# Performance work log

Hardware: AMD Instinct MI355X
Metric: run time of the kernel (lower is better)

## Reference

```python
import jax, jax.numpy as jnp
import numpy as np


def setup_inputs() -> dict:
    key = jax.random.key(0)
    kx, ky = jax.random.split(key)
    B, N, M, D = 4, 8192, 8192, 3
    x = jax.random.normal(kx, (B, N, D), dtype=jnp.float32)
    y = jax.random.normal(ky, (B, M, D), dtype=jnp.float32)
    return {"x": x, "y": y}


def reference(x, y):
    # Pairwise squared distances: [B, N, M]
    x2 = jnp.sum(x * x, axis=-1)  # [B, N]
    y2 = jnp.sum(y * y, axis=-1)  # [B, M]
    xy = jnp.einsum("bnd,bmd->bnm", x, y)  # [B, N, M]
    d2 = x2[:, :, None] + y2[:, None, :] - 2.0 * xy
    # Chamfer: min over the other set in each direction
    min_xy = jnp.min(d2, axis=2)  # [B, N] nearest y for each x
    min_yx = jnp.min(d2, axis=1)  # [B, M] nearest x for each y
    return jnp.mean(min_xy) + jnp.mean(min_yx)
```

## Files before the change

### kernel.cpp

```cpp
#include <hip/hip_runtime.h>

#define BATCHES 4
#define NPTS    8192
#define INF32   3.0e38f

typedef _Float16 f16x8  __attribute__((ext_vector_type(8)));
typedef float    f32x16 __attribute__((ext_vector_type(16)));

__device__ inline void fsplit(float v, _Float16& h, _Float16& l) {
    h = (_Float16)v;
    l = (_Float16)(v - (float)h);
}

__device__ inline void pack_point(float p0, float p1, float p2,
                                  _Float16* __restrict__ avec,
                                  _Float16* __restrict__ bvec)
{
    _Float16 h[3], l[3];
    fsplit(p0, h[0], l[0]); fsplit(p1, h[1], l[1]); fsplit(p2, h[2], l[2]);
    float q = fmaf(p2, p2, fmaf(p1, p1, p0 * p0));
    _Float16 qh, ql;
    fsplit(q, qh, ql);

    __align__(16) _Float16 av[16];
    __align__(16) _Float16 bv[16];
    #pragma unroll
    for (int k = 0; k < 3; ++k) {
        av[k]     = h[k];
        av[3 + k] = l[k];
        av[6 + k] = h[k];
        bv[k]     = (_Float16)(-2.0f * (float)h[k]);
        bv[3 + k] = bv[k];
        bv[6 + k] = (_Float16)(-2.0f * (float)l[k]);
    }
    av[9] = qh; av[10] = ql; av[11] = (_Float16)1.0f; av[12] = (_Float16)1.0f;
    bv[9] = (_Float16)1.0f; bv[10] = (_Float16)1.0f; bv[11] = qh; bv[12] = ql;
    av[13] = av[14] = av[15] = (_Float16)0.0f;
    bv[13] = bv[14] = bv[15] = (_Float16)0.0f;

    ((int4*)avec)[0] = ((int4*)av)[0]; ((int4*)avec)[1] = ((int4*)av)[1];
    ((int4*)bvec)[0] = ((int4*)bv)[0]; ((int4*)bvec)[1] = ((int4*)bv)[1];
}

__global__ __launch_bounds__(256) void chamfer_prep(
    const float* __restrict__ x, const float* __restrict__ y,
    _Float16* __restrict__ pAx, _Float16* __restrict__ pBx,
    _Float16* __restrict__ pAy, _Float16* __restrict__ pBy,
    int* __restrict__ mininit )
{
    int i = blockIdx.x * 256 + threadIdx.x;
    mininit[i]         = 0x7F7F7F7F;
    mininit[i + 32768] = 0x7F7F7F7F;

    const float* xp = x + (size_t)i * 3;
    const float* yp = y + (size_t)i * 3;
    pack_point(xp[0], xp[1], xp[2], pAx + (size_t)i * 16, pBx + (size_t)i * 16);
    pack_point(yp[0], yp[1], yp[2], pAy + (size_t)i * 16, pBy + (size_t)i * 16);
}

__global__ __launch_bounds__(256, 4) void chamfer_mfma(
    const _Float16* __restrict__ pAx, const _Float16* __restrict__ pBx,
    const _Float16* __restrict__ pAy, const _Float16* __restrict__ pBy,
    float* __restrict__ minall )
{
    int bid   = blockIdx.x;
    int dir   = bid >> 9;
    int rem   = bid & 511;
    int b     = rem >> 7;
    int rem2  = rem & 127;
    int strip = rem2 >> 2;
    int chunk = rem2 & 3;
    int tid   = threadIdx.x;
    int wv    = tid >> 6, lane = tid & 63;
    int lo    = lane & 31, hi = lane >> 5;

    const _Float16* Adata = ((dir == 0) ? pAx : pAy) + (size_t)b * NPTS * 16;
    const _Float16* Bdata = ((dir == 0) ? pBy : pBx) + (size_t)b * NPTS * 16;
    float* outMin = minall + ((size_t)dir << 15) + (size_t)b * NPTS;

    int rw = strip * 256 + wv * 64;
    int c0 = chunk * 2048;

    f16x8 af0 = *(const f16x8*)(Adata + (size_t)(rw + lo) * 16 + hi * 8);
    f16x8 af1 = *(const f16x8*)(Adata + (size_t)(rw + 32 + lo) * 16 + hi * 8);

    float rmin0[16], rmin1[16];
    #pragma unroll
    for (int r = 0; r < 16; ++r) { rmin0[r] = INF32; rmin1[r] = INF32; }

    const f32x16 zero = {0.f,0.f,0.f,0.f,0.f,0.f,0.f,0.f,
                         0.f,0.f,0.f,0.f,0.f,0.f,0.f,0.f};

    auto loadB = [&](int t) -> f16x8 {
        return *(const f16x8*)(Bdata + (size_t)(c0 + (t << 5) + lo) * 16 + hi * 8);
    };

    f16x8 b0 = loadB(0), b1 = loadB(1);
    #pragma unroll 1
    for (int t = 0; t < 64; t += 2) {
        f16x8 n0 = loadB((t + 2) & 63);
        f16x8 n1 = loadB((t + 3) & 63);
        f32x16 A0 = __builtin_amdgcn_mfma_f32_32x32x16_f16(af0, b0, zero, 0, 0, 0);
        f32x16 A1 = __builtin_amdgcn_mfma_f32_32x32x16_f16(af0, b1, zero, 0, 0, 0);
        #pragma unroll
        for (int r = 0; r < 16; ++r)
            rmin0[r] = fminf(fminf(A0[r], A1[r]), rmin0[r]);
        f32x16 B0 = __builtin_amdgcn_mfma_f32_32x32x16_f16(af1, b0, zero, 0, 0, 0);
        f32x16 B1 = __builtin_amdgcn_mfma_f32_32x32x16_f16(af1, b1, zero, 0, 0, 0);
        #pragma unroll
        for (int r = 0; r < 16; ++r)
            rmin1[r] = fminf(fminf(B0[r], B1[r]), rmin1[r]);
        b0 = n0; b1 = n1;
    }

    #pragma unroll
    for (int r = 0; r < 16; ++r) {
        float v = rmin0[r];
        v = fminf(v, __shfl_xor(v, 1, 64));
        v = fminf(v, __shfl_xor(v, 2, 64));
        v = fminf(v, __shfl_xor(v, 4, 64));
        v = fminf(v, __shfl_xor(v, 8, 64));
        v = fminf(v, __shfl_xor(v, 16, 64));
        float w = rmin1[r];
        w = fminf(w, __shfl_xor(w, 1, 64));
        w = fminf(w, __shfl_xor(w, 2, 64));
        w = fminf(w, __shfl_xor(w, 4, 64));
        w = fminf(w, __shfl_xor(w, 8, 64));
        w = fminf(w, __shfl_xor(w, 16, 64));
        if (lo == 0) {
            int rr = (r & 3) + ((r >> 2) << 3) + (hi << 2);
            atomicMin((int*)&outMin[rw + rr],
                      __float_as_int(fmaxf(v, 0.f)));
            atomicMin((int*)&outMin[rw + 32 + rr],
                      __float_as_int(fmaxf(w, 0.f)));
        }
    }
}

__global__ __launch_bounds__(256) void chamfer_reduce1(
    const float* __restrict__ minbuf, double* __restrict__ partials)
{
    int base = blockIdx.x * 1024 + threadIdx.x * 4;
    float4 v = *reinterpret_cast<const float4*>(minbuf + base);
    double s = ((double)v.x + (double)v.y) + ((double)v.z + (double)v.w);
    #pragma unroll
    for (int off = 32; off > 0; off >>= 1) s += __shfl_down(s, off, 64);
    __shared__ double sd[4];
    int wid = threadIdx.x >> 6;
    if ((threadIdx.x & 63) == 0) sd[wid] = s;
    __syncthreads();
    if (threadIdx.x == 0)
        partials[blockIdx.x] = (sd[0] + sd[1]) + (sd[2] + sd[3]);
}

__global__ __launch_bounds__(64) void chamfer_reduce2(
    const double* __restrict__ partials, float* __restrict__ out)
{
    double s = partials[threadIdx.x];
    #pragma unroll
    for (int off = 32; off > 0; off >>= 1) s += __shfl_down(s, off, 64);
    if (threadIdx.x == 0)
        out[0] = (float)(s / (double)(BATCHES * NPTS));
}

extern "C" void kernel_launch(void* const* d_in, const int* in_sizes, int n_in,
                              void* d_out, int out_size, void* d_ws, size_t ws_size,
                              hipStream_t stream)
{
    const float* x = (const float*)d_in[0];
    const float* y = (const float*)d_in[1];
    float* out = (float*)d_out;

    float*    minall = (float*)d_ws;
    _Float16* pAx = (_Float16*)(minall + 65536);
    _Float16* pBx = pAx + (size_t)BATCHES * NPTS * 16;
    _Float16* pAy = pBx + (size_t)BATCHES * NPTS * 16;
    _Float16* pBy = pAy + (size_t)BATCHES * NPTS * 16;
    double*   partials = (double*)(pBy + (size_t)BATCHES * NPTS * 16);

    chamfer_prep<<<BATCHES * NPTS / 256, 256, 0, stream>>>(
        x, y, pAx, pBx, pAy, pBy, (int*)minall);
    chamfer_mfma<<<1024, 256, 0, stream>>>(pAx, pBx, pAy, pBy, minall);
    chamfer_reduce1<<<64, 256, 0, stream>>>(minall, partials);
    chamfer_reduce2<<<1, 64, 0, stream>>>(partials, out);
}
```

Before: 39.37 us.

## Software-pipeline MFMA min-reduction with one row tile per wave

Each wave now owns a single 32-row A tile and covers 4096 columns instead of two row tiles over 2048 columns. The loop is restructured so the min-reduction of the previous MFMA results overlaps with issuing the next MFMAs, using two sets of accumulators and B loads prefetched two steps ahead. The aim is to hide MFMA latency behind VALU min work and halve the atomics per wave. The cost is twice the B-operand loads per MFMA, since B tiles are no longer shared across two A tiles.

```diff
diff --git a/kernel.cpp b/kernel.cpp
--- a/kernel.cpp
+++ b/kernel.cpp
@@ -68,8 +68,8 @@
     int rem   = bid & 511;
     int b     = rem >> 7;
     int rem2  = rem & 127;
-    int strip = rem2 >> 2;
-    int chunk = rem2 & 3;
+    int strip = rem2 >> 1;
+    int chunk = rem2 & 1;
     int tid   = threadIdx.x;
     int wv    = tid >> 6, lane = tid & 63;
     int lo    = lane & 31, hi = lane >> 5;
@@ -78,15 +78,14 @@
     const _Float16* Bdata = ((dir == 0) ? pBy : pBx) + (size_t)b * NPTS * 16;
     float* outMin = minall + ((size_t)dir << 15) + (size_t)b * NPTS;
 
-    int rw = strip * 256 + wv * 64;
-    int c0 = chunk * 2048;
+    int rw = strip * 128 + wv * 32;
+    int c0 = chunk * 4096;
 
-    f16x8 af0 = *(const f16x8*)(Adata + (size_t)(rw + lo) * 16 + hi * 8);
-    f16x8 af1 = *(const f16x8*)(Adata + (size_t)(rw + 32 + lo) * 16 + hi * 8);
+    f16x8 af = *(const f16x8*)(Adata + (size_t)(rw + lo) * 16 + hi * 8);
 
-    float rmin0[16], rmin1[16];
+    float rmin[16];
     #pragma unroll
-    for (int r = 0; r < 16; ++r) { rmin0[r] = INF32; rmin1[r] = INF32; }
+    for (int r = 0; r < 16; ++r) rmin[r] = INF32;
 
     const f32x16 zero = {0.f,0.f,0.f,0.f,0.f,0.f,0.f,0.f,
                          0.f,0.f,0.f,0.f,0.f,0.f,0.f,0.f};
@@ -95,44 +94,51 @@
         return *(const f16x8*)(Bdata + (size_t)(c0 + (t << 5) + lo) * 16 + hi * 8);
     };
 
-    f16x8 b0 = loadB(0), b1 = loadB(1);
+#define MIN16(P0, P1)                                                  \
+    _Pragma("unroll")                                                  \
+    for (int r = 0; r < 16; ++r)                                       \
+        rmin[r] = fminf(fminf(P0[r], P1[r]), rmin[r]);
+
+    f16x8 bA0 = loadB(0), bA1 = loadB(1), bB0 = loadB(2), bB1 = loadB(3);
+    f32x16 R0 = __builtin_amdgcn_mfma_f32_32x32x16_f16(af, bA0, zero, 0, 0, 0);
+    f32x16 R1 = __builtin_amdgcn_mfma_f32_32x32x16_f16(af, bA1, zero, 0, 0, 0);
+    f32x16 S0 = __builtin_amdgcn_mfma_f32_32x32x16_f16(af, bB0, zero, 0, 0, 0);
+    f32x16 S1 = __builtin_amdgcn_mfma_f32_32x32x16_f16(af, bB1, zero, 0, 0, 0);
+    bA0 = loadB(4); bA1 = loadB(5); bB0 = loadB(6); bB1 = loadB(7);
+
     #pragma unroll 1
-    for (int t = 0; t < 64; t += 2) {
-        f16x8 n0 = loadB((t + 2) & 63);
-        f16x8 n1 = loadB((t + 3) & 63);
-        f32x16 A0 = __builtin_amdgcn_mfma_f32_32x32x16_f16(af0, b0, zero, 0, 0, 0);
-        f32x16 A1 = __builtin_amdgcn_mfma_f32_32x32x16_f16(af0, b1, zero, 0, 0, 0);
-        #pragma unroll
-        for (int r = 0; r < 16; ++r)
-            rmin0[r] = fminf(fminf(A0[r], A1[r]), rmin0[r]);
-        f32x16 B0 = __builtin_amdgcn_mfma_f32_32x32x16_f16(af1, b0, zero, 0, 0, 0);
-        f32x16 B1 = __builtin_amdgcn_mfma_f32_32x32x16_f16(af1, b1, zero, 0, 0, 0);
-        #pragma unroll
-        for (int r = 0; r < 16; ++r)
-            rmin1[r] = fminf(fminf(B0[r], B1[r]), rmin1[r]);
-        b0 = n0; b1 = n1;
+    for (int p = 0; p < 30; ++p) {
+        MIN16(R0, R1)
+        R0 = __builtin_amdgcn_mfma_f32_32x32x16_f16(af, bA0, zero, 0, 0, 0);
+        R1 = __builtin_amdgcn_mfma_f32_32x32x16_f16(af, bA1, zero, 0, 0, 0);
+        bA0 = loadB(4 * p + 8); bA1 = loadB(4 * p + 9);
+        MIN16(S0, S1)
+        S0 = __builtin_amdgcn_mfma_f32_32x32x16_f16(af, bB0, zero, 0, 0, 0);
+        S1 = __builtin_amdgcn_mfma_f32_32x32x16_f16(af, bB1, zero, 0, 0, 0);
+        bB0 = loadB(4 * p + 10); bB1 = loadB(4 * p + 11);
     }
+
+    MIN16(R0, R1)
+    R0 = __builtin_amdgcn_mfma_f32_32x32x16_f16(af, bA0, zero, 0, 0, 0);
+    R1 = __builtin_amdgcn_mfma_f32_32x32x16_f16(af, bA1, zero, 0, 0, 0);
+    MIN16(S0, S1)
+    S0 = __builtin_amdgcn_mfma_f32_32x32x16_f16(af, bB0, zero, 0, 0, 0);
+    S1 = __builtin_amdgcn_mfma_f32_32x32x16_f16(af, bB1, zero, 0, 0, 0);
+    MIN16(R0, R1)
+    MIN16(S0, S1)
+#undef MIN16
 
     #pragma unroll
     for (int r = 0; r < 16; ++r) {
-        float v = rmin0[r];
+        float v = rmin[r];
         v = fminf(v, __shfl_xor(v, 1, 64));
         v = fminf(v, __shfl_xor(v, 2, 64));
         v = fminf(v, __shfl_xor(v, 4, 64));
         v = fminf(v, __shfl_xor(v, 8, 64));
         v = fminf(v, __shfl_xor(v, 16, 64));
-        float w = rmin1[r];
-        w = fminf(w, __shfl_xor(w, 1, 64));
-        w = fminf(w, __shfl_xor(w, 2, 64));
-        w = fminf(w, __shfl_xor(w, 4, 64));
-        w = fminf(w, __shfl_xor(w, 8, 64));
-        w = fminf(w, __shfl_xor(w, 16, 64));
         if (lo == 0) {
             int rr = (r & 3) + ((r >> 2) << 3) + (hi << 2);
-            atomicMin((int*)&outMin[rw + rr],
-                      __float_as_int(fmaxf(v, 0.f)));
-            atomicMin((int*)&outMin[rw + 32 + rr],
-                      __float_as_int(fmaxf(w, 0.f)));
+            atomicMin((int*)&outMin[rw + rr], __float_as_int(fmaxf(v, 0.f)));
         }
     }
 }
```

After: 126.4 us. +221.1%, slower.

## Stage B column chunk in LDS shared across eight waves per block

Applied to the files above, without the earlier changes.

Blocks grow from 256 to 512 threads, each covering 512 rows instead of 256, and the grid is halved. The 2048-point B chunk (64 KB of fp16) is cooperatively loaded into shared memory once per block, and the MFMA loop reads B fragments from LDS instead of global memory. This cuts redundant global/L2 traffic for B across waves. The cost is a 64 KB LDS allocation that limits blocks per CU, plus a barrier before compute with no overlap of the initial load.

```diff
diff --git a/kernel.cpp b/kernel.cpp
--- a/kernel.cpp
+++ b/kernel.cpp
@@ -58,16 +58,16 @@
     pack_point(yp[0], yp[1], yp[2], pAy + (size_t)i * 16, pBy + (size_t)i * 16);
 }
 
-__global__ __launch_bounds__(256, 4) void chamfer_mfma(
+__global__ __launch_bounds__(512, 4) void chamfer_mfma(
     const _Float16* __restrict__ pAx, const _Float16* __restrict__ pBx,
     const _Float16* __restrict__ pAy, const _Float16* __restrict__ pBy,
     float* __restrict__ minall )
 {
     int bid   = blockIdx.x;
-    int dir   = bid >> 9;
-    int rem   = bid & 511;
-    int b     = rem >> 7;
-    int rem2  = rem & 127;
+    int dir   = bid >> 8;
+    int rem   = bid & 255;
+    int b     = rem >> 6;
+    int rem2  = rem & 63;
     int strip = rem2 >> 2;
     int chunk = rem2 & 3;
     int tid   = threadIdx.x;
@@ -78,8 +78,18 @@
     const _Float16* Bdata = ((dir == 0) ? pBy : pBx) + (size_t)b * NPTS * 16;
     float* outMin = minall + ((size_t)dir << 15) + (size_t)b * NPTS;
 
-    int rw = strip * 256 + wv * 64;
+    int rw = strip * 512 + wv * 64;
     int c0 = chunk * 2048;
+
+    __shared__ __align__(16) _Float16 sB[64 * 512];
+    #pragma unroll
+    for (int tt = 0; tt < 8; ++tt) {
+        int t = wv + tt * 8;
+        const int4* src = (const int4*)(Bdata +
+            ((size_t)(c0 + (t << 5) + lo) << 4) + (hi << 3));
+        *(int4*)(sB + (size_t)t * 512 + lane * 8) = *src;
+    }
+    __syncthreads();
 
     f16x8 af0 = *(const f16x8*)(Adata + (size_t)(rw + lo) * 16 + hi * 8);
     f16x8 af1 = *(const f16x8*)(Adata + (size_t)(rw + 32 + lo) * 16 + hi * 8);
@@ -91,26 +101,26 @@
     const f32x16 zero = {0.f,0.f,0.f,0.f,0.f,0.f,0.f,0.f,
                          0.f,0.f,0.f,0.f,0.f,0.f,0.f,0.f};
 
-    auto loadB = [&](int t) -> f16x8 {
-        return *(const f16x8*)(Bdata + (size_t)(c0 + (t << 5) + lo) * 16 + hi * 8);
+    auto ldsB = [&](int t) -> f16x8 {
+        return *(const f16x8*)(sB + ((size_t)(t & 63) << 9) + lane * 8);
     };
 
-    f16x8 b0 = loadB(0), b1 = loadB(1);
+    f16x8 bc0 = ldsB(0), bc1 = ldsB(1);
     #pragma unroll 1
     for (int t = 0; t < 64; t += 2) {
-        f16x8 n0 = loadB((t + 2) & 63);
-        f16x8 n1 = loadB((t + 3) & 63);
-        f32x16 A0 = __builtin_amdgcn_mfma_f32_32x32x16_f16(af0, b0, zero, 0, 0, 0);
-        f32x16 A1 = __builtin_amdgcn_mfma_f32_32x32x16_f16(af0, b1, zero, 0, 0, 0);
+        f16x8 nb0 = ldsB(t + 2);
+        f16x8 nb1 = ldsB(t + 3);
+        f32x16 A0 = __builtin_amdgcn_mfma_f32_32x32x16_f16(af0, bc0, zero, 0, 0, 0);
+        f32x16 A1 = __builtin_amdgcn_mfma_f32_32x32x16_f16(af0, bc1, zero, 0, 0, 0);
         #pragma unroll
         for (int r = 0; r < 16; ++r)
             rmin0[r] = fminf(fminf(A0[r], A1[r]), rmin0[r]);
-        f32x16 B0 = __builtin_amdgcn_mfma_f32_32x32x16_f16(af1, b0, zero, 0, 0, 0);
-        f32x16 B1 = __builtin_amdgcn_mfma_f32_32x32x16_f16(af1, b1, zero, 0, 0, 0);
+        f32x16 B0 = __builtin_amdgcn_mfma_f32_32x32x16_f16(af1, bc0, zero, 0, 0, 0);
+        f32x16 B1 = __builtin_amdgcn_mfma_f32_32x32x16_f16(af1, bc1, zero, 0, 0, 0);
         #pragma unroll
         for (int r = 0; r < 16; ++r)
             rmin1[r] = fminf(fminf(B0[r], B1[r]), rmin1[r]);
-        b0 = n0; b1 = n1;
+        bc0 = nb0; bc1 = nb1;
     }
 
     #pragma unroll
@@ -129,10 +139,8 @@
         w = fminf(w, __shfl_xor(w, 16, 64));
         if (lo == 0) {
             int rr = (r & 3) + ((r >> 2) << 3) + (hi << 2);
-            atomicMin((int*)&outMin[rw + rr],
-                      __float_as_int(fmaxf(v, 0.f)));
-            atomicMin((int*)&outMin[rw + 32 + rr],
-                      __float_as_int(fmaxf(w, 0.f)));
+            atomicMin((int*)&outMin[rw + rr],      __float_as_int(fmaxf(v, 0.f)));
+            atomicMin((int*)&outMin[rw + 32 + rr], __float_as_int(fmaxf(w, 0.f)));
         }
     }
 }
@@ -180,7 +188,7 @@
 
     chamfer_prep<<<BATCHES * NPTS / 256, 256, 0, stream>>>(
         x, y, pAx, pBx, pAy, pBy, (int*)minall);
-    chamfer_mfma<<<1024, 256, 0, stream>>>(pAx, pBx, pAy, pBy, minall);
+    chamfer_mfma<<<512, 512, 0, stream>>>(pAx, pBx, pAy, pBy, minall);
     chamfer_reduce1<<<64, 256, 0, stream>>>(minall, partials);
     chamfer_reduce2<<<1, 64, 0, stream>>>(partials, out);
 }
```

Measured after the change: 36.53 us. 7.2% less time.
